# Kernel optimization log

Hardware: AMD Instinct MI355X
Metric: run time of the kernel (lower is better)

The kernel has to match this reference:

```python
import jax, jax.numpy as jnp
import numpy as np

B, T, E = 8, 2048, 2048

def setup_inputs() -> dict:
    key = jax.random.key(0)
    k1, k2, k3 = jax.random.split(key, 3)
    x = jax.random.normal(k1, (B, T, E), dtype=jnp.float32)
    weight = jax.random.normal(k2, (T,), dtype=jnp.float32)
    bias = jax.random.normal(k3, (T,), dtype=jnp.float32)
    return {"x": x, "weight": weight, "bias": bias}

def _toeplitz_matrix(v, T):
    # M[i, j] = v[j - i] for j >= i, else 0  (upper-triangular Toeplitz)
    idx = jnp.arange(T)
    diff = idx[None, :] - idx[:, None]          # [T, T], diff = j - i
    M = jnp.where(diff >= 0, v[jnp.clip(diff, 0, T - 1)], jnp.zeros((), v.dtype))
    return M

def reference(x, weight, bias):
    Tlen = x.shape[1]
    W = _toeplitz_matrix(weight[:Tlen], Tlen).astype(x.dtype)  # [T, T]
    # original: out[b,e,t'] = sum_t x[b,e,t] * W[t,t']; in (B,T,E) layout:
    out = jnp.einsum('bte,ts->bse', x, W)
    out = out + bias[:Tlen][None, :, None]
    return out
```

## Files before the change

kernel.cpp:

```cpp
#include <hip/hip_runtime.h>
#include <hip/hip_bf16.h>

#define T_LEN 2048
#define E_LEN 2048
#define B_SZ  8
#define BM 128
#define BN 128
#define BK2 64
#define WREV_LEN 4104

typedef short short8 __attribute__((ext_vector_type(8)));
typedef float floatx4 __attribute__((ext_vector_type(4)));

typedef const __attribute__((address_space(1))) void* gas_ptr;
typedef __attribute__((address_space(3))) void* lds_ptr;

__global__ __launch_bounds__(256) void transpose_cast(
    const float* __restrict__ x, __hip_bfloat16* __restrict__ xT)
{
    const int t0 = blockIdx.x * 64, e0 = blockIdx.y * 64, b = blockIdx.z;
    __shared__ unsigned int W[64][33];
    const int tid = threadIdx.x;
    const int wave = tid >> 6, lane = tid & 63;

    const float* xb = x + (size_t)b * T_LEN * E_LEN;
    const int c = tid & 15;
    const int q = tid >> 4;

    #pragma unroll
    for (int i = 0; i < 2; ++i) {
        const int tp = q + 16 * i;
        const float4 a4 = *reinterpret_cast<const float4*>(
            xb + (size_t)(t0 + 2 * tp) * E_LEN + e0 + 4 * c);
        const float4 b4 = *reinterpret_cast<const float4*>(
            xb + (size_t)(t0 + 2 * tp + 1) * E_LEN + e0 + 4 * c);
        const float av[4] = {a4.x, a4.y, a4.z, a4.w};
        const float bv[4] = {b4.x, b4.y, b4.z, b4.w};
        #pragma unroll
        for (int j = 0; j < 4; ++j) {
            __hip_bfloat16 ha = __float2bfloat16(av[j]);
            __hip_bfloat16 hb = __float2bfloat16(bv[j]);
            unsigned int w =
                (unsigned int)*reinterpret_cast<unsigned short*>(&ha) |
                ((unsigned int)*reinterpret_cast<unsigned short*>(&hb) << 16);
            W[4 * c + j][tp] = w;
        }
    }
    __syncthreads();

    __hip_bfloat16* xTb = xT + (size_t)b * E_LEN * T_LEN;
    const int er = lane >> 3;
    const int pc = (lane & 7) * 4;
    #pragma unroll
    for (int i = 0; i < 2; ++i) {
        const int e = wave * 8 + i * 32 + er;
        uint4 v;
        v.x = W[e][pc + 0];
        v.y = W[e][pc + 1];
        v.z = W[e][pc + 2];
        v.w = W[e][pc + 3];
        unsigned int* dst =
            reinterpret_cast<unsigned int*>(xTb + (size_t)(e0 + e) * T_LEN + t0);
        *reinterpret_cast<uint4*>(dst + pc) = v;
    }
}

__global__ __launch_bounds__(256) void build_wrevs(
    const float* __restrict__ w, __hip_bfloat16* __restrict__ wrevs)
{
    int total = 8 * WREV_LEN;
    for (int i = threadIdx.x + blockIdx.x * blockDim.x; i < total;
         i += blockDim.x * gridDim.x) {
        int p = i / WREV_LEN, q = i - p * WREV_LEN;
        int j = q + p;
        float v = (j < T_LEN) ? w[T_LEN - 1 - j] : 0.0f;
        wrevs[i] = __float2bfloat16(v);
    }
}

__global__ __launch_bounds__(256) void toeplitz_gemm(
    const __hip_bfloat16* __restrict__ xT,
    const __hip_bfloat16* __restrict__ wrevs,
    const float* __restrict__ bias,
    float* __restrict__ out)
{
    const int bx = blockIdx.x;
    const int mb = bx & 15, b = bx >> 4;
    const int nb = 15 - (int)blockIdx.y;
    const int e0 = mb * BM, s0 = nb * BN;
    const int tid = threadIdx.x;
    const int wave = tid >> 6, lane = tid & 63;
    const int wm = (wave & 1) * 64;
    const int wn = (wave >> 1) * 64;
    const int ln15 = lane & 15, quad = lane >> 4;

    __shared__ __hip_bfloat16 Atile[2][BM][BK2];

    floatx4 acc[4][4];
    #pragma unroll
    for (int i = 0; i < 4; ++i)
        #pragma unroll
        for (int j = 0; j < 4; ++j)
            acc[i][j] = (floatx4){0.f, 0.f, 0.f, 0.f};

    const int ktiles = (s0 + BN) / BK2;
    const __hip_bfloat16* xTb = xT + ((size_t)b * E_LEN + e0) * T_LEN;
    const short* wr = reinterpret_cast<const short*>(wrevs);
    char* AtileB = reinterpret_cast<char*>(&Atile[0][0][0]);

    auto STAGE = [&](int buf, int kt) {
        const int t0 = kt * BK2;
        #pragma unroll
        for (int j = 0; j < 4; ++j) {
            const int c0 = (wave * 4 + j) * 64;
            const int c  = c0 + lane;
            const int r  = c >> 3, p = c & 7;
            const int ps = p ^ (r & 7);
            const __hip_bfloat16* g = xTb + (size_t)r * T_LEN + t0 + ps * 8;
            __builtin_amdgcn_global_load_lds(
                (gas_ptr)g,
                (lds_ptr)(AtileB + (size_t)buf * (BM * BK2 * 2) + c0 * 16),
                16, 0, 0);
        }
    };

    STAGE(0, 0);
    __syncthreads();
    int cur = 0;

    for (int kt = 0; kt < ktiles; ++kt) {
        if (kt + 1 < ktiles) STAGE(cur ^ 1, kt + 1);
        const int t0 = kt * BK2;
        const char* Abuf = AtileB + (size_t)cur * (BM * BK2 * 2);

        #pragma unroll
        for (int kk = 0; kk < 2; ++kk) {
            short8 bfrag[4];
            #pragma unroll
            for (int ni = 0; ni < 4; ++ni) {
                int s = s0 + wn + ni * 16 + ln15;
                int C = (T_LEN - 1) - s + t0 + kk * 32 + quad * 8;
                int p = C & 7;
                bfrag[ni] = *reinterpret_cast<const short8*>(
                    wr + (size_t)p * WREV_LEN + (C - p));
            }
            short8 afrag[4];
            const int q = kk * 4 + quad;
            #pragma unroll
            for (int mi = 0; mi < 4; ++mi) {
                int r = wm + mi * 16 + ln15;
                int chunk = r * 8 + (q ^ (r & 7));
                afrag[mi] = *reinterpret_cast<const short8*>(Abuf + chunk * 16);
            }
            #pragma unroll
            for (int mi = 0; mi < 4; ++mi)
                #pragma unroll
                for (int ni = 0; ni < 4; ++ni)
                    acc[mi][ni] = __builtin_amdgcn_mfma_f32_16x16x32_bf16(
                        afrag[mi], bfrag[ni], acc[mi][ni], 0, 0, 0);
        }
        __syncthreads();
        cur ^= 1;
    }

    #pragma unroll
    for (int ni = 0; ni < 4; ++ni) {
        int s = s0 + wn + ni * 16 + ln15;
        float bv = bias[s];
        #pragma unroll
        for (int mi = 0; mi < 4; ++mi) {
            int e = e0 + wm + mi * 16 + quad * 4;
            float* dst = out + ((size_t)b * T_LEN + s) * E_LEN + e;
            floatx4 v = acc[mi][ni];
            v.x += bv; v.y += bv; v.z += bv; v.w += bv;
            *reinterpret_cast<floatx4*>(dst) = v;
        }
    }
}

extern "C" void kernel_launch(void* const* d_in, const int* in_sizes, int n_in,
                              void* d_out, int out_size, void* d_ws, size_t ws_size,
                              hipStream_t stream)
{
    const float* x    = (const float*)d_in[0];
    const float* w    = (const float*)d_in[1];
    const float* bias = (const float*)d_in[2];
    float* out = (float*)d_out;

    __hip_bfloat16* xT = (__hip_bfloat16*)d_ws;
    __hip_bfloat16* wrevs =
        (__hip_bfloat16*)((char*)d_ws + (size_t)B_SZ * E_LEN * T_LEN * 2);

    transpose_cast<<<dim3(T_LEN / 64, E_LEN / 64, B_SZ), 256, 0, stream>>>(x, xT);
    build_wrevs<<<dim3(64), 256, 0, stream>>>(w, wrevs);
    toeplitz_gemm<<<dim3(16 * B_SZ, 16), 256, 0, stream>>>(xT, wrevs, bias, out);
}
```

Baseline: 316.8 us.

## Rewrite Toeplitz GEMM with 256x256 tiles, LDS-resident weights, triple-buffered ping-pong phases

The GEMM kernel moves to 256x256 output tiles with 512 threads (8 waves, each computing 128x64). The reversed-weight Toeplitz band for the tile is preloaded into LDS instead of being read from global memory every k-step. The A tiles are triple-buffered with prefetch two steps ahead, and each k-step is split into four MFMA phases with barriers and s_setprio so that loads and math from different waves interleave. The grid is remapped to 1D with a swizzle across blocks. This raises register and LDS use per block (about 130KB LDS, 128 accumulator registers), which may limit occupancy. The triangular load imbalance now comes in coarser 256-wide chunks.

```diff
diff --git a/kernel.cpp b/kernel.cpp
--- a/kernel.cpp
+++ b/kernel.cpp
@@ -4,10 +4,13 @@
 #define T_LEN 2048
 #define E_LEN 2048
 #define B_SZ  8
-#define BM 128
-#define BN 128
+#define BM 256
+#define BN 256
 #define BK2 64
 #define WREV_LEN 4104
+#define CL 2312
+#define ABUF_B 32768
+#define BOFF (3 * ABUF_B)
 
 typedef short short8 __attribute__((ext_vector_type(8)));
 typedef float floatx4 __attribute__((ext_vector_type(4)));
@@ -78,98 +81,155 @@
     }
 }
 
-__global__ __launch_bounds__(256) void toeplitz_gemm(
+#define LOAD_A(MH)                                                             \
+    _Pragma("unroll")                                                          \
+    for (int m4 = 0; m4 < 4; ++m4) {                                           \
+        const int r = arow + ((MH) * 4 + m4) * 16;                             \
+        afr[m4][0] = *reinterpret_cast<const short8*>(Ab + r * 128 + xq0 * 16);\
+        afr[m4][1] = *reinterpret_cast<const short8*>(Ab + r * 128 + xq1 * 16);\
+    }
+
+#define LOAD_B(NH)                                                             \
+    _Pragma("unroll")                                                          \
+    for (int n2 = 0; n2 < 2; ++n2) {                                           \
+        _Pragma("unroll")                                                      \
+        for (int kk = 0; kk < 2; ++kk) {                                       \
+            const int C = Cb + t0 + kk * 32 - ((NH) * 2 + n2) * 16;            \
+            const int p = C & 7;                                               \
+            bfr[n2][kk] = *reinterpret_cast<const short8*>(                    \
+                L + BOFF + p * (CL * 2) + ((C - p) - Wbase) * 2);              \
+        }                                                                      \
+    }
+
+#define MFMA16(MH, NH)                                                         \
+    _Pragma("unroll")                                                          \
+    for (int kk = 0; kk < 2; ++kk)                                             \
+        _Pragma("unroll")                                                      \
+        for (int m4 = 0; m4 < 4; ++m4)                                         \
+            _Pragma("unroll")                                                  \
+            for (int n2 = 0; n2 < 2; ++n2)                                     \
+                acc[(MH) * 4 + m4][(NH) * 2 + n2] =                            \
+                    __builtin_amdgcn_mfma_f32_16x16x32_bf16(                   \
+                        afr[m4][kk], bfr[n2][kk],                              \
+                        acc[(MH) * 4 + m4][(NH) * 2 + n2], 0, 0, 0);
+
+#define PHASE_SYNC_PRE()                                                       \
+    __builtin_amdgcn_s_barrier();                                              \
+    asm volatile("s_waitcnt lgkmcnt(0)" ::: "memory");                         \
+    __builtin_amdgcn_sched_barrier(0);                                         \
+    __builtin_amdgcn_s_setprio(1);
+
+#define PHASE_SYNC_POST()                                                      \
+    __builtin_amdgcn_s_setprio(0);                                             \
+    __builtin_amdgcn_s_barrier();
+
+__global__ __launch_bounds__(512, 2) void toeplitz_gemm(
     const __hip_bfloat16* __restrict__ xT,
     const __hip_bfloat16* __restrict__ wrevs,
     const float* __restrict__ bias,
     float* __restrict__ out)
 {
-    const int bx = blockIdx.x;
-    const int mb = bx & 15, b = bx >> 4;
-    const int nb = 15 - (int)blockIdx.y;
+    __shared__ __align__(16) char L[3 * ABUF_B + 8 * CL * 2];
+
+    const int bid = blockIdx.x;
+    const int lid = (bid & 7) * 64 + (bid >> 3);
+    const int nb = 7 - (lid & 7);
+    const int panel = lid >> 3;
+    const int mb = panel & 7, b = panel >> 3;
     const int e0 = mb * BM, s0 = nb * BN;
     const int tid = threadIdx.x;
     const int wave = tid >> 6, lane = tid & 63;
-    const int wm = (wave & 1) * 64;
-    const int wn = (wave >> 1) * 64;
-    const int ln15 = lane & 15, quad = lane >> 4;
-
-    __shared__ __hip_bfloat16 Atile[2][BM][BK2];
-
-    floatx4 acc[4][4];
-    #pragma unroll
-    for (int i = 0; i < 4; ++i)
+    const int wm = (wave >> 2) * 128;
+    const int wn = (wave & 3) * 64;
+    const int ln15 = lane & 15, quad = lane >> 4, ln7 = lane & 7;
+
+    const int ktiles = (s0 + BN) / BK2;
+    const int Wbase = T_LEN - 264 - s0;
+    const __hip_bfloat16* xTb = xT + ((size_t)b * E_LEN + e0) * T_LEN;
+
+    for (int i = tid; i < 8 * (CL / 8); i += 512) {
+        const int p = i / (CL / 8), c = i - p * (CL / 8);
+        int q = Wbase + c * 8;
+        if (q < 0) q = 0;
+        const uint4 v = *(reinterpret_cast<const uint4*>(
+            wrevs + (size_t)p * WREV_LEN + q));
+        *(reinterpret_cast<uint4*>(L + BOFF + (size_t)p * (CL * 2)) + c) = v;
+    }
+    __syncthreads();
+
+    floatx4 acc[8][4];
+    #pragma unroll
+    for (int i = 0; i < 8; ++i)
         #pragma unroll
         for (int j = 0; j < 4; ++j)
             acc[i][j] = (floatx4){0.f, 0.f, 0.f, 0.f};
 
-    const int ktiles = (s0 + BN) / BK2;
-    const __hip_bfloat16* xTb = xT + ((size_t)b * E_LEN + e0) * T_LEN;
-    const short* wr = reinterpret_cast<const short*>(wrevs);
-    char* AtileB = reinterpret_cast<char*>(&Atile[0][0][0]);
-
-    auto STAGE = [&](int buf, int kt) {
+    auto STAGE1 = [&](int buf, int kt2, int cc) {
+        const int t0n = kt2 * BK2;
+        const int c = cc * 512 + tid;
+        const int r = c >> 3, p = c & 7;
+        const int ps = p ^ (r & 7);
+        const __hip_bfloat16* g = xTb + (size_t)r * T_LEN + t0n + ps * 8;
+        __builtin_amdgcn_global_load_lds(
+            (gas_ptr)g,
+            (lds_ptr)(L + buf * ABUF_B + (cc * 512 + wave * 64) * 16), 16, 0, 0);
+    };
+
+    STAGE1(0, 0, 0); STAGE1(0, 0, 1); STAGE1(0, 0, 2); STAGE1(0, 0, 3);
+    STAGE1(1, 1, 0); STAGE1(1, 1, 1); STAGE1(1, 1, 2); STAGE1(1, 1, 3);
+    asm volatile("s_waitcnt vmcnt(4)" ::: "memory");
+    __builtin_amdgcn_s_barrier();
+
+    const int arow = wm + ln15;
+    const int xq0 = quad ^ ln7;
+    const int xq1 = (4 + quad) ^ ln7;
+    const int Cb = (T_LEN - 1 - s0 - wn - ln15) + quad * 8;
+
+    short8 afr[4][2], bfr[2][2];
+    int bi = 0;
+    for (int kt = 0; kt < ktiles; ++kt) {
         const int t0 = kt * BK2;
+        const char* Ab = L + bi * ABUF_B;
+        const int pf = (kt + 2 < ktiles);
+        const int bp = (bi + 2 >= 3) ? bi - 1 : bi + 2;
+
+        LOAD_A(0) LOAD_B(0)
+        if (pf) STAGE1(bp, kt + 2, 0);
+        PHASE_SYNC_PRE()
+        MFMA16(0, 0)
+        PHASE_SYNC_POST()
+
+        LOAD_A(1)
+        if (pf) STAGE1(bp, kt + 2, 1);
+        PHASE_SYNC_PRE()
+        MFMA16(1, 0)
+        PHASE_SYNC_POST()
+
+        LOAD_B(1)
+        if (pf) STAGE1(bp, kt + 2, 2);
+        PHASE_SYNC_PRE()
+        MFMA16(1, 1)
+        PHASE_SYNC_POST()
+
+        LOAD_A(0)
+        if (pf) STAGE1(bp, kt + 2, 3);
+        PHASE_SYNC_PRE()
+        MFMA16(0, 1)
+        __builtin_amdgcn_s_setprio(0);
+        if (pf) asm volatile("s_waitcnt vmcnt(4)" ::: "memory");
+        else    asm volatile("s_waitcnt vmcnt(0)" ::: "memory");
+        __builtin_amdgcn_s_barrier();
+
+        bi = (bi + 1 == 3) ? 0 : bi + 1;
+    }
+
+    #pragma unroll
+    for (int ni = 0; ni < 4; ++ni) {
+        const int s = s0 + wn + ni * 16 + ln15;
+        const float bv = bias[s];
         #pragma unroll
-        for (int j = 0; j < 4; ++j) {
-            const int c0 = (wave * 4 + j) * 64;
-            const int c  = c0 + lane;
-            const int r  = c >> 3, p = c & 7;
-            const int ps = p ^ (r & 7);
-            const __hip_bfloat16* g = xTb + (size_t)r * T_LEN + t0 + ps * 8;
-            __builtin_amdgcn_global_load_lds(
-                (gas_ptr)g,
-                (lds_ptr)(AtileB + (size_t)buf * (BM * BK2 * 2) + c0 * 16),
-                16, 0, 0);
-        }
-    };
-
-    STAGE(0, 0);
-    __syncthreads();
-    int cur = 0;
-
-    for (int kt = 0; kt < ktiles; ++kt) {
-        if (kt + 1 < ktiles) STAGE(cur ^ 1, kt + 1);
-        const int t0 = kt * BK2;
-        const char* Abuf = AtileB + (size_t)cur * (BM * BK2 * 2);
-
-        #pragma unroll
-        for (int kk = 0; kk < 2; ++kk) {
-            short8 bfrag[4];
-            #pragma unroll
-            for (int ni = 0; ni < 4; ++ni) {
-                int s = s0 + wn + ni * 16 + ln15;
-                int C = (T_LEN - 1) - s + t0 + kk * 32 + quad * 8;
-                int p = C & 7;
-                bfrag[ni] = *reinterpret_cast<const short8*>(
-                    wr + (size_t)p * WREV_LEN + (C - p));
-            }
-            short8 afrag[4];
-            const int q = kk * 4 + quad;
-            #pragma unroll
-            for (int mi = 0; mi < 4; ++mi) {
-                int r = wm + mi * 16 + ln15;
-                int chunk = r * 8 + (q ^ (r & 7));
-                afrag[mi] = *reinterpret_cast<const short8*>(Abuf + chunk * 16);
-            }
-            #pragma unroll
-            for (int mi = 0; mi < 4; ++mi)
-                #pragma unroll
-                for (int ni = 0; ni < 4; ++ni)
-                    acc[mi][ni] = __builtin_amdgcn_mfma_f32_16x16x32_bf16(
-                        afrag[mi], bfrag[ni], acc[mi][ni], 0, 0, 0);
-        }
-        __syncthreads();
-        cur ^= 1;
-    }
-
-    #pragma unroll
-    for (int ni = 0; ni < 4; ++ni) {
-        int s = s0 + wn + ni * 16 + ln15;
-        float bv = bias[s];
-        #pragma unroll
-        for (int mi = 0; mi < 4; ++mi) {
-            int e = e0 + wm + mi * 16 + quad * 4;
+        for (int mi = 0; mi < 8; ++mi) {
+            const int e = e0 + wm + mi * 16 + quad * 4;
             float* dst = out + ((size_t)b * T_LEN + s) * E_LEN + e;
             floatx4 v = acc[mi][ni];
             v.x += bv; v.y += bv; v.z += bv; v.w += bv;
@@ -193,5 +253,5 @@
 
     transpose_cast<<<dim3(T_LEN / 64, E_LEN / 64, B_SZ), 256, 0, stream>>>(x, xT);
     build_wrevs<<<dim3(64), 256, 0, stream>>>(w, wrevs);
-    toeplitz_gemm<<<dim3(16 * B_SZ, 16), 256, 0, stream>>>(xT, wrevs, bias, out);
-}
+    toeplitz_gemm<<<dim3(512), 512, 0, stream>>>(xT, wrevs, bias, out);
+}
```

Measured after the change: 346.4 us. 1.09x slower.
